# Kernel optimization log

Measured on AMD Instinct MI355X. Metric: run time of the kernel, lower is better.

## Reference

```python
import jax, jax.numpy as jnp
import numpy as np

B, S, D, H = 2, 4096, 512, 8
HD = D // H  # 64


def setup_inputs() -> dict:
    key = jax.random.key(0)
    ks = jax.random.split(key, 9)
    def lin_init(kw, kb, fan_in, fan_out):
        bound = 1.0 / np.sqrt(fan_in)
        W = jax.random.uniform(kw, (fan_in, fan_out), minval=-bound, maxval=bound, dtype=jnp.float32)
        b = jax.random.uniform(kb, (fan_out,), minval=-bound, maxval=bound, dtype=jnp.float32)
        return W, b
    Wq, bq = lin_init(ks[0], ks[1], D, D)
    Wk, bk = lin_init(ks[2], ks[3], D, D)
    Wv, bv = lin_init(ks[4], ks[5], D, D)
    query = jax.random.normal(ks[6], (B, S, D), dtype=jnp.float32)
    key_in = jax.random.normal(ks[7], (B, S, D), dtype=jnp.float32)
    value = jax.random.normal(ks[8], (B, S, D), dtype=jnp.float32)
    return {"query": query, "key": key_in, "value": value,
            "Wq": Wq, "bq": bq, "Wk": Wk, "bk": bk, "Wv": Wv, "bv": bv}


def _split_heads(x):
    # [B, S, D] -> [B, H, S, HD]
    b, s, _ = x.shape
    return x.reshape(b, s, H, HD).transpose(0, 2, 1, 3)


def reference(query, key, value, Wq, bq, Wk, bk, Wv, bv):
    Q = _split_heads(query @ Wq + bq)
    K = _split_heads(key @ Wk + bk)
    V = _split_heads(value @ Wv + bv)
    scale = 1.0 / np.sqrt(HD).astype(np.float32)
    # scores: [B, H, Sq, Sk]
    scores = jnp.einsum('bhqd,bhkd->bhqk', Q, K) * scale
    weights = jax.nn.softmax(scores, axis=-1)
    att = jnp.einsum('bhqk,bhkd->bhqd', weights, V)
    # [B, H, S, HD] -> [B, S, D]
    return att.transpose(0, 2, 1, 3).reshape(query.shape[0], query.shape[1], D)
```

## Files before the change

### kernel.cpp

```cpp
#include <hip/hip_runtime.h>
#include <hip/hip_bf16.h>
#include <cstdint>


typedef __bf16   bf16x8 __attribute__((ext_vector_type(8)));
typedef _Float16 f16x8  __attribute__((ext_vector_type(8)));
typedef _Float16 f16x2  __attribute__((ext_vector_type(2)));
typedef float    f32x4  __attribute__((ext_vector_type(4)));
typedef float    f32x16 __attribute__((ext_vector_type(16)));
typedef unsigned int   u32;
typedef unsigned int   u32x4 __attribute__((ext_vector_type(4)));
typedef unsigned short u16;

#define NB  2
#define SEQ 4096
#define DIM 512
#define NH  8
#define HD  64
#define WSZ (DIM * DIM)
#define XSZ (NB * SEQ * DIM)
#define QSZ (NB * NH * SEQ * HD)

#if __has_builtin(__builtin_amdgcn_fdot2)
#define HAVE_FDOT2 1
#else
#define HAVE_FDOT2 0
#endif

__device__ __forceinline__ u16 f2bf(float f) {
    __bf16 h = (__bf16)f; return __builtin_bit_cast(u16, h);
}
__device__ __forceinline__ u16 f2h(float f) {
    _Float16 h = (_Float16)f; return __builtin_bit_cast(u16, h);
}
__device__ __forceinline__ u32 pack_pkrtz(float a, float b) {
    auto pk = __builtin_amdgcn_cvt_pkrtz(a, b);
    return __builtin_bit_cast(u32, pk);
}
__device__ __forceinline__ bf16x8 cvt8p(float4 a, float4 b) {
    bf16x8 o;
    o[0]=(__bf16)a.x; o[1]=(__bf16)a.y; o[2]=(__bf16)a.z; o[3]=(__bf16)a.w;
    o[4]=(__bf16)b.x; o[5]=(__bf16)b.y; o[6]=(__bf16)b.z; o[7]=(__bf16)b.w;
    return o;
}
__device__ __forceinline__ void dma16(const u16* g, u16* l) {
    __builtin_amdgcn_global_load_lds(
        (const __attribute__((address_space(1))) u32*)g,
        (__attribute__((address_space(3))) u32*)l, 16, 0, 0);
}

__global__ __launch_bounds__(256) void prep_kernel(
    const float* __restrict__ xq, const float* __restrict__ xk,
    const float* __restrict__ xv,
    const float* __restrict__ Wq, const float* __restrict__ Wk,
    const float* __restrict__ Wv,
    u16* __restrict__ xb, u16* __restrict__ wtImg)
{
    __shared__ u16 lT[64 * 65];
    const int id = blockIdx.x;
    const int t = threadIdx.x;
    if (id < 3072) {
        const int p = id >> 10, rest = id & 1023;
        const int mtile = rest >> 4, kk = rest & 15;
        const float* X = (p == 0) ? xq : ((p == 1) ? xk : xv);
        const int row = t >> 1, half = t & 1;
        const float* src = X + ((size_t)(mtile * 128 + row)) * DIM + kk * 32 + half * 16;
        u16* dst = xb + (size_t)p * XSZ + ((size_t)(mtile * 16 + kk)) * 4096 + row * 32;
        const int sr = (row ^ (row >> 2)) & 3;
        float4 a0 = ((const float4*)src)[0], a1 = ((const float4*)src)[1];
        float4 a2 = ((const float4*)src)[2], a3 = ((const float4*)src)[3];
        const int c0 = (half * 2) ^ sr, c1 = (half * 2 + 1) ^ sr;
        *(bf16x8*)(dst + (c0 << 3)) = cvt8p(a0, a1);
        *(bf16x8*)(dst + (c1 << 3)) = cvt8p(a2, a3);
    } else {
        const int id2 = id - 3072;
        const int p = id2 >> 6;
        const float* W = (p == 0) ? Wq : ((p == 1) ? Wk : Wv);
        const int r0 = ((id2 >> 3) & 7) * 64, c0 = (id2 & 7) * 64;
#pragma unroll
        for (int i = 0; i < 16; i++) {
            int idx = i * 256 + t, rowk = idx >> 6, coln = idx & 63;
            lT[coln * 65 + rowk] = f2bf(W[(size_t)(r0 + rowk) * DIM + c0 + coln]);
        }
        __syncthreads();
#pragma unroll
        for (int i = 0; i < 2; i++) {
            const int idx = i * 256 + t;
            const int nl = idx >> 3, ch = idx & 7;
            const int n = c0 + nl;
            const int row = n & 127, ntile = n >> 7;
            const int kk = (r0 >> 5) + (ch >> 2);
            const int sw = (ch & 3) ^ ((row ^ (row >> 2)) & 3);
            u16* d = wtImg + (size_t)p * WSZ + ((size_t)(ntile * 16 + kk)) * 4096
                   + row * 32 + (sw << 3);
#pragma unroll
            for (int e = 0; e < 8; e++) d[e] = lT[nl * 65 + ch * 8 + e];
        }
    }
}

__global__ __launch_bounds__(256) void proj_kernel(
    const u16* __restrict__ xb, const u16* __restrict__ wtImg,
    const float* __restrict__ bq, const float* __restrict__ bk,
    const float* __restrict__ bv,
    u16* __restrict__ qb, u16* __restrict__ kbImg, u16* __restrict__ vtImg)
{
    __shared__ u16 smem[16384];

    const int tid = threadIdx.x;
    const int wave = tid >> 6, lane = tid & 63;
    const int l16 = lane & 15, quad = lane >> 4;
    const int wq = wave >> 1, wn = wave & 1;

    const int id = blockIdx.x;
    const int xcd = id & 7, j = id >> 3;
    const int p = j >> 5, t5 = j & 31;
    int mb, nb;
    if (p < 2) { mb = xcd * 8 + (t5 >> 2); nb = t5 & 3; }
    else       { nb = xcd * 8 + (t5 >> 2); mb = t5 & 3; }

    const u16* Abase = (p < 2) ? xb + (size_t)p * XSZ + (size_t)mb * 16 * 4096
                               : wtImg + (size_t)2 * WSZ + (size_t)mb * 16 * 4096;
    const u16* Bbase = (p < 2) ? wtImg + (size_t)p * WSZ + (size_t)nb * 16 * 4096
                               : xb + (size_t)2 * XSZ + (size_t)nb * 16 * 4096;
    const int doff = tid * 8;

    f32x4 acc[4][4];
#pragma unroll
    for (int ms = 0; ms < 4; ms++)
#pragma unroll
        for (int ns = 0; ns < 4; ns++)
#pragma unroll
            for (int jj = 0; jj < 4; jj++) acc[ms][ns][jj] = 0.f;

#pragma unroll
    for (int e = 0; e < 2; e++) {
        dma16(Abase + e * 2048 + doff, smem + e * 2048 + doff);
        dma16(Bbase + e * 2048 + doff, smem + 4096 + e * 2048 + doff);
    }
    Abase += 4096; Bbase += 4096;

    for (int kt = 0; kt < 16; kt++) {
        __syncthreads();
        if (kt < 15) {
            u16* lb = smem + ((kt + 1) & 1) * 8192;
#pragma unroll
            for (int e = 0; e < 2; e++) {
                dma16(Abase + e * 2048 + doff, lb + e * 2048 + doff);
                dma16(Bbase + e * 2048 + doff, lb + 4096 + e * 2048 + doff);
            }
            Abase += 4096; Bbase += 4096;
        }
        const u16* lA = smem + (kt & 1) * 8192;
        const u16* lB = lA + 4096;

        bf16x8 af[4];
#pragma unroll
        for (int ms = 0; ms < 4; ms++) {
            const int row = wq * 64 + ms * 16 + l16;
            const int sr = (row ^ (row >> 2)) & 3;
            af[ms] = *(const bf16x8*)&lA[row * 32 + ((quad ^ sr) << 3)];
        }
#pragma unroll
        for (int ns = 0; ns < 4; ns++) {
            const int rowb = wn * 64 + ns * 16 + l16;
            const int sb = (rowb ^ (rowb >> 2)) & 3;
            const bf16x8 b = *(const bf16x8*)&lB[rowb * 32 + ((quad ^ sb) << 3)];
#pragma unroll
            for (int ms = 0; ms < 4; ms++)
                acc[ms][ns] = __builtin_amdgcn_mfma_f32_16x16x32_bf16(af[ms], b, acc[ms][ns], 0, 0, 0);
        }
    }

    __syncthreads();
    if (p < 2) {
        const float* bias = p ? bk : bq;
        const float cs = (p == 0) ? 0.18033688011112042f : 1.0f;
        const int stl = wn * 2 + wq;
        const int hh = nb * 2 + wn;
#pragma unroll
        for (int ns = 0; ns < 4; ns++) {
            const int ch = ns * 16 + l16;
            const float bval = bias[hh * 64 + ch];
#pragma unroll
            for (int ms = 0; ms < 4; ms++)
#pragma unroll
                for (int rr = 0; rr < 4; rr++) {
                    const int sqL = ms * 16 + quad * 4 + rr;
                    const float v = (acc[ms][ns][rr] + bval) * cs;
                    int off;
                    if (p == 0) off = sqL * 64 + ch;
                    else        off = sqL * 64 +
                                      (((ch >> 3) ^ ((sqL ^ (sqL >> 3)) & 7)) << 3) + (ch & 7);
                    smem[stl * 4096 + off] = f2bf(v);
                }
        }
    } else {
        const int stl = wq * 2 + wn;
#pragma unroll
        for (int ms = 0; ms < 4; ms++)
#pragma unroll
            for (int rr = 0; rr < 4; rr++) {
                const int hd = ms * 16 + quad * 4 + rr;
                const float bval = bv[mb * 128 + wq * 64 + hd];
                const int swh = (hd ^ (hd >> 3)) & 7;
#pragma unroll
                for (int ns = 0; ns < 4; ns++) {
                    const int nl = ns * 16 + l16;
                    const int sqpL = (nl & ~12) | ((nl & 8) >> 1) | ((nl & 4) << 1);
                    smem[stl * 4096 + hd * 64 +
                         (((sqpL >> 3) ^ swh) << 3) + (sqpL & 7)] =
                        f2h(acc[ms][ns][rr] + bval);
                }
            }
    }
    __syncthreads();

    {
        u16* dstp; size_t gbase;
        if (p < 2) {
            const int hh = nb * 2 + (wave >> 1);
            const int b2 = mb >> 5;
            const int row0 = (mb * 128 + (wave & 1) * 64) & 4095;
            if (p == 0) { dstp = qb;    gbase = ((size_t)(b2 * NH + hh) * 4096 + row0) * 64; }
            else        { dstp = kbImg; gbase = ((size_t)((b2 * NH + hh) * 64 + (row0 >> 6))) * 4096; }
        } else {
            const int hh = mb * 2 + (wave >> 1);
            const int b2 = nb >> 5;
            const int nblk = (nb & 31) * 2 + (wave & 1);
            dstp = vtImg; gbase = ((size_t)((b2 * NH + hh) * 64 + nblk)) * 4096;
        }
#pragma unroll
        for (int e = 0; e < 8; e++) {
            const u32x4 vv = *(const u32x4*)&smem[wave * 4096 + e * 512 + lane * 8];
            *(u32x4*)(dstp + gbase + e * 512 + lane * 8) = vv;
        }
    }
}

__global__ __launch_bounds__(512, 4) void attn_kernel(
    const u16* __restrict__ qb, const u16* __restrict__ kbImg,
    const u16* __restrict__ vtImg, float* __restrict__ out)
{
    __shared__ u16 smem[2 * 4 * 4096];
    float* cmb = (float*)smem;

    const int tid = threadIdx.x;
    const int wave = tid >> 6, lane = tid & 63;
    const int m31 = lane & 31, h = lane >> 5;
    const int wq = wave >> 1, kh = wave & 1;

    const int blk = blockIdx.x;
    const int xcd = blk & 7, idx = blk >> 3;
    const int bh = xcd * 2 + (idx >> 5);
    const int qt = idx & 31;
    const int qbase = qt * 128 + wq * 32;

    bf16x8 qF[4];
#pragma unroll
    for (int c = 0; c < 4; c++)
        qF[c] = *(const bf16x8*)(qb + ((size_t)bh * SEQ + qbase + m31) * HD + c * 16 + h * 8);

    f32x16 O0, O1;
#pragma unroll
    for (int j = 0; j < 16; j++) { O0[j] = 0.f; O1[j] = 0.f; }
    float la_ = 0.f, lb_ = 0.f;
#if HAVE_FDOT2
    const f16x2 one2 = {(_Float16)1.f, (_Float16)1.f};
#endif

    const int st  = wave >> 1;
    const int hw  = wave & 1;
    const u16* img = (st & 1) ? vtImg : kbImg;
    const u16* gp = img + ((size_t)(bh * 64 + (st >> 1) * 32)) * 4096 + hw * 2048 + lane * 8;
    {
        u16* lb = smem + st * 4096 + hw * 2048 + lane * 8;
#pragma unroll
        for (int e = 0; e < 4; e++) dma16(gp + e * 512, lb + e * 512);
        gp += 4096;
    }

    const int swV0 = (m31 ^ (m31 >> 3)) & 7;
    const int rV1  = 32 + m31;
    const int swV1 = (rV1 ^ (rV1 >> 3)) & 7;
    const int rK0  = m31;
    const int swK0 = (rK0 ^ (rK0 >> 3)) & 7;
    const int rK1  = 32 + m31;
    const int swK1 = (rK1 ^ (rK1 >> 3)) & 7;

    const int NT = 32;
    for (int it = 0; it < NT; it++) {
        __syncthreads();
        if (it + 1 < NT) {
            u16* lb = smem + ((((it + 1) & 1) * 4 + st)) * 4096 + hw * 2048 + lane * 8;
#pragma unroll
            for (int e = 0; e < 4; e++) dma16(gp + e * 512, lb + e * 512);
            gp += 4096;
        }
        const u16* sK = smem + (size_t)(((it & 1) * 4) + kh * 2) * 4096;
        const u16* sV = sK + 4096;

        bf16x8 kA0[4];
#pragma unroll
        for (int c = 0; c < 4; c++)
            kA0[c] = *(const bf16x8*)&sK[(rK0 << 6) + (((2 * c + h) ^ swK0) << 3)];

        f32x16 Sv0;
#pragma unroll
        for (int j = 0; j < 16; j++) Sv0[j] = 0.f;
        __builtin_amdgcn_s_setprio(1);
#pragma unroll
        for (int c = 0; c < 4; c++)
            Sv0 = __builtin_amdgcn_mfma_f32_32x32x16_bf16(kA0[c], qF[c], Sv0, 0, 0, 0);
        __builtin_amdgcn_s_setprio(0);

        f16x8 vA00[2], vA01[2];
#pragma unroll
        for (int c2 = 0; c2 < 2; c2++) {
            vA00[c2] = *(const f16x8*)&sV[(m31 << 6) + (((2 * c2 + h) ^ swV0) << 3)];
            vA01[c2] = *(const f16x8*)&sV[(rV1 << 6) + (((2 * c2 + h) ^ swV1) << 3)];
        }

        u32 P0[8];
#pragma unroll
        for (int mm = 0; mm < 8; mm++) {
            const float ea = __builtin_amdgcn_exp2f(Sv0[2 * mm]);
            const float eb = __builtin_amdgcn_exp2f(Sv0[2 * mm + 1]);
            P0[mm] = pack_pkrtz(ea, eb);
#if HAVE_FDOT2
            const f16x2 pp = __builtin_bit_cast(f16x2, P0[mm]);
            if (mm & 1) lb_ = __builtin_amdgcn_fdot2(pp, one2, lb_, false);
            else        la_ = __builtin_amdgcn_fdot2(pp, one2, la_, false);
#else
            if (mm & 1) lb_ += ea + eb; else la_ += ea + eb;
#endif
        }
        u32x4 g0, g1;
        g0[0] = P0[0]; g0[1] = P0[1]; g0[2] = P0[2]; g0[3] = P0[3];
        g1[0] = P0[4]; g1[1] = P0[5]; g1[2] = P0[6]; g1[3] = P0[7];
        const f16x8 pf00 = __builtin_bit_cast(f16x8, g0);
        const f16x8 pf01 = __builtin_bit_cast(f16x8, g1);

        bf16x8 kA1[4];
#pragma unroll
        for (int c = 0; c < 4; c++)
            kA1[c] = *(const bf16x8*)&sK[(rK1 << 6) + (((2 * c + h) ^ swK1) << 3)];

        f32x16 Sv1;
#pragma unroll
        for (int j = 0; j < 16; j++) Sv1[j] = 0.f;

        __builtin_amdgcn_s_setprio(1);
        Sv1 = __builtin_amdgcn_mfma_f32_32x32x16_bf16(kA1[0], qF[0], Sv1, 0, 0, 0);
        O0  = __builtin_amdgcn_mfma_f32_32x32x16_f16(vA00[0], pf00, O0, 0, 0, 0);
        Sv1 = __builtin_amdgcn_mfma_f32_32x32x16_bf16(kA1[1], qF[1], Sv1, 0, 0, 0);
        O0  = __builtin_amdgcn_mfma_f32_32x32x16_f16(vA00[1], pf01, O0, 0, 0, 0);
        Sv1 = __builtin_amdgcn_mfma_f32_32x32x16_bf16(kA1[2], qF[2], Sv1, 0, 0, 0);
        O1  = __builtin_amdgcn_mfma_f32_32x32x16_f16(vA01[0], pf00, O1, 0, 0, 0);
        Sv1 = __builtin_amdgcn_mfma_f32_32x32x16_bf16(kA1[3], qF[3], Sv1, 0, 0, 0);
        O1  = __builtin_amdgcn_mfma_f32_32x32x16_f16(vA01[1], pf01, O1, 0, 0, 0);
        __builtin_amdgcn_s_setprio(0);

        f16x8 vA10[2], vA11[2];
#pragma unroll
        for (int c2 = 0; c2 < 2; c2++) {
            vA10[c2] = *(const f16x8*)&sV[(m31 << 6) + (((4 + 2 * c2 + h) ^ swV0) << 3)];
            vA11[c2] = *(const f16x8*)&sV[(rV1 << 6) + (((4 + 2 * c2 + h) ^ swV1) << 3)];
        }

        u32 P1[8];
#pragma unroll
        for (int mm = 0; mm < 8; mm++) {
            const float ea = __builtin_amdgcn_exp2f(Sv1[2 * mm]);
            const float eb = __builtin_amdgcn_exp2f(Sv1[2 * mm + 1]);
            P1[mm] = pack_pkrtz(ea, eb);
#if HAVE_FDOT2
            const f16x2 pp = __builtin_bit_cast(f16x2, P1[mm]);
            if (mm & 1) lb_ = __builtin_amdgcn_fdot2(pp, one2, lb_, false);
            else        la_ = __builtin_amdgcn_fdot2(pp, one2, la_, false);
#else
            if (mm & 1) lb_ += ea + eb; else la_ += ea + eb;
#endif
        }
        u32x4 h0, h1;
        h0[0] = P1[0]; h0[1] = P1[1]; h0[2] = P1[2]; h0[3] = P1[3];
        h1[0] = P1[4]; h1[1] = P1[5]; h1[2] = P1[6]; h1[3] = P1[7];
        const f16x8 pf10 = __builtin_bit_cast(f16x8, h0);
        const f16x8 pf11 = __builtin_bit_cast(f16x8, h1);

        __builtin_amdgcn_s_setprio(1);
        O0 = __builtin_amdgcn_mfma_f32_32x32x16_f16(vA10[0], pf10, O0, 0, 0, 0);
        O0 = __builtin_amdgcn_mfma_f32_32x32x16_f16(vA10[1], pf11, O0, 0, 0, 0);
        O1 = __builtin_amdgcn_mfma_f32_32x32x16_f16(vA11[0], pf10, O1, 0, 0, 0);
        O1 = __builtin_amdgcn_mfma_f32_32x32x16_f16(vA11[1], pf11, O1, 0, 0, 0);
        __builtin_amdgcn_s_setprio(0);
    }

    float l_acc = la_ + lb_;
    l_acc += __shfl_xor(l_acc, 32);
    __syncthreads();
    if (kh == 1) {
#pragma unroll
        for (int hg = 0; hg < 2; hg++)
#pragma unroll
            for (int mm = 0; mm < 4; mm++) {
                f32x4 o;
#pragma unroll
                for (int j = 0; j < 4; j++) o[j] = (hg ? O1 : O0)[4 * mm + j];
                *(f32x4*)&cmb[(((wq * 2 + hg) * 4 + mm) << 8) + lane * 4] = o;
            }
        cmb[8192 + wq * 64 + lane] = l_acc;
    }
    __syncthreads();

    if (kh == 0) {
        const int b = bh >> 3, hcol = bh & 7;
        const float lt = l_acc + cmb[8192 + wq * 64 + lane];
        const float inv = 1.0f / lt;
        const int sq = qbase + m31;
#pragma unroll
        for (int hg = 0; hg < 2; hg++)
#pragma unroll
            for (int mm = 0; mm < 4; mm++) {
                const f32x4 po = *(const f32x4*)&cmb[(((wq * 2 + hg) * 4 + mm) << 8) + lane * 4];
                f32x4 o;
#pragma unroll
                for (int j = 0; j < 4; j++)
                    o[j] = ((hg ? O1 : O0)[4 * mm + j] + po[j]) * inv;
                *(f32x4*)&out[(((size_t)(b * SEQ + sq)) << 9) + hcol * 64
                              + hg * 32 + 8 * mm + 4 * h] = o;
            }
    }
}

extern "C" void kernel_launch(void* const* d_in, const int* in_sizes, int n_in,
                              void* d_out, int out_size, void* d_ws, size_t ws_size,
                              hipStream_t stream)
{
    const float* q  = (const float*)d_in[0];
    const float* k  = (const float*)d_in[1];
    const float* v  = (const float*)d_in[2];
    const float* Wq = (const float*)d_in[3];
    const float* bq = (const float*)d_in[4];
    const float* Wk = (const float*)d_in[5];
    const float* bk = (const float*)d_in[6];
    const float* Wv = (const float*)d_in[7];
    const float* bv = (const float*)d_in[8];
    float* out = (float*)d_out;

    u16* xb  = (u16*)d_ws;
    u16* wti = xb  + (size_t)3 * XSZ;
    u16* qbp = wti + (size_t)3 * WSZ;
    u16* kbp = qbp + (size_t)QSZ;
    u16* vtp = kbp + (size_t)QSZ;

    prep_kernel<<<dim3(3264), 256, 0, stream>>>(q, k, v, Wq, Wk, Wv, xb, wti);
    proj_kernel<<<dim3(768),  256, 0, stream>>>(xb, wti, bq, bk, bv,
                                                qbp, kbp, vtp);
    attn_kernel<<<dim3(512),  512, 0, stream>>>(qbp, kbp, vtp, out);
}
```

Before: 202.5 us.

## Fuse fp32-to-bf16 activation conversion into projection GEMM loads

The prep kernel no longer converts the three fp32 activation tensors to a swizzled bf16 image in workspace. The projection kernel now reads fp32 activations directly with register loads, converts them, and writes them into LDS after the MFMA work of each k-step, while weights still stream in via global_load_lds DMA. This removes a full write-then-read round trip of the bf16 activation copy and shrinks the prep launch to the weight transpose only. In exchange, the GEMM loop reads twice as many bytes for activations, holds more registers, and does conversion work inside the loop.

```diff
diff --git a/kernel.cpp b/kernel.cpp
--- a/kernel.cpp
+++ b/kernel.cpp
@@ -18,7 +18,6 @@
 #define NH  8
 #define HD  64
 #define WSZ (DIM * DIM)
-#define XSZ (NB * SEQ * DIM)
 #define QSZ (NB * NH * SEQ * HD)
 
 #if __has_builtin(__builtin_amdgcn_fdot2)
@@ -49,58 +48,39 @@
         (__attribute__((address_space(3))) u32*)l, 16, 0, 0);
 }
 
-__global__ __launch_bounds__(256) void prep_kernel(
-    const float* __restrict__ xq, const float* __restrict__ xk,
-    const float* __restrict__ xv,
+__global__ __launch_bounds__(256) void wt_kernel(
     const float* __restrict__ Wq, const float* __restrict__ Wk,
-    const float* __restrict__ Wv,
-    u16* __restrict__ xb, u16* __restrict__ wtImg)
+    const float* __restrict__ Wv, u16* __restrict__ wtImg)
 {
     __shared__ u16 lT[64 * 65];
-    const int id = blockIdx.x;
+    const int p = blockIdx.z;
+    const float* W = (p == 0) ? Wq : ((p == 1) ? Wk : Wv);
+    const int r0 = blockIdx.x * 64, c0 = blockIdx.y * 64;
     const int t = threadIdx.x;
-    if (id < 3072) {
-        const int p = id >> 10, rest = id & 1023;
-        const int mtile = rest >> 4, kk = rest & 15;
-        const float* X = (p == 0) ? xq : ((p == 1) ? xk : xv);
-        const int row = t >> 1, half = t & 1;
-        const float* src = X + ((size_t)(mtile * 128 + row)) * DIM + kk * 32 + half * 16;
-        u16* dst = xb + (size_t)p * XSZ + ((size_t)(mtile * 16 + kk)) * 4096 + row * 32;
-        const int sr = (row ^ (row >> 2)) & 3;
-        float4 a0 = ((const float4*)src)[0], a1 = ((const float4*)src)[1];
-        float4 a2 = ((const float4*)src)[2], a3 = ((const float4*)src)[3];
-        const int c0 = (half * 2) ^ sr, c1 = (half * 2 + 1) ^ sr;
-        *(bf16x8*)(dst + (c0 << 3)) = cvt8p(a0, a1);
-        *(bf16x8*)(dst + (c1 << 3)) = cvt8p(a2, a3);
-    } else {
-        const int id2 = id - 3072;
-        const int p = id2 >> 6;
-        const float* W = (p == 0) ? Wq : ((p == 1) ? Wk : Wv);
-        const int r0 = ((id2 >> 3) & 7) * 64, c0 = (id2 & 7) * 64;
-#pragma unroll
-        for (int i = 0; i < 16; i++) {
-            int idx = i * 256 + t, rowk = idx >> 6, coln = idx & 63;
-            lT[coln * 65 + rowk] = f2bf(W[(size_t)(r0 + rowk) * DIM + c0 + coln]);
-        }
-        __syncthreads();
-#pragma unroll
-        for (int i = 0; i < 2; i++) {
-            const int idx = i * 256 + t;
-            const int nl = idx >> 3, ch = idx & 7;
-            const int n = c0 + nl;
-            const int row = n & 127, ntile = n >> 7;
-            const int kk = (r0 >> 5) + (ch >> 2);
-            const int sw = (ch & 3) ^ ((row ^ (row >> 2)) & 3);
-            u16* d = wtImg + (size_t)p * WSZ + ((size_t)(ntile * 16 + kk)) * 4096
-                   + row * 32 + (sw << 3);
-#pragma unroll
-            for (int e = 0; e < 8; e++) d[e] = lT[nl * 65 + ch * 8 + e];
-        }
+#pragma unroll
+    for (int i = 0; i < 16; i++) {
+        int idx = i * 256 + t, rowk = idx >> 6, coln = idx & 63;
+        lT[coln * 65 + rowk] = f2bf(W[(size_t)(r0 + rowk) * DIM + c0 + coln]);
+    }
+    __syncthreads();
+#pragma unroll
+    for (int i = 0; i < 2; i++) {
+        const int idx = i * 256 + t;
+        const int nl = idx >> 3, ch = idx & 7;
+        const int n = c0 + nl;
+        const int row = n & 127, ntile = n >> 7;
+        const int kk = (r0 >> 5) + (ch >> 2);
+        const int sw = (ch & 3) ^ ((row ^ (row >> 2)) & 3);
+        u16* d = wtImg + (size_t)p * WSZ + ((size_t)(ntile * 16 + kk)) * 4096
+               + row * 32 + (sw << 3);
+#pragma unroll
+        for (int e = 0; e < 8; e++) d[e] = lT[nl * 65 + ch * 8 + e];
     }
 }
 
 __global__ __launch_bounds__(256) void proj_kernel(
-    const u16* __restrict__ xb, const u16* __restrict__ wtImg,
+    const float* __restrict__ xq, const float* __restrict__ xk,
+    const float* __restrict__ xv, const u16* __restrict__ wtImg,
     const float* __restrict__ bq, const float* __restrict__ bk,
     const float* __restrict__ bv,
     u16* __restrict__ qb, u16* __restrict__ kbImg, u16* __restrict__ vtImg)
@@ -119,10 +99,17 @@
     if (p < 2) { mb = xcd * 8 + (t5 >> 2); nb = t5 & 3; }
     else       { nb = xcd * 8 + (t5 >> 2); mb = t5 & 3; }
 
-    const u16* Abase = (p < 2) ? xb + (size_t)p * XSZ + (size_t)mb * 16 * 4096
+    const float* Xp = (p == 0) ? xq : ((p == 1) ? xk : xv);
+    const int xtile = (p < 2) ? mb : nb;
+    const int row = tid >> 1, half = tid & 1;
+    const int sr = (row ^ (row >> 2)) & 3;
+    const float* xsrc = Xp + (size_t)(xtile * 128 + row) * DIM + half * 16;
+    const int xldsoff = (p < 2) ? 0 : 4096;
+    const int c0 = (((half * 2) ^ sr) << 3), c1 = (((half * 2 + 1) ^ sr) << 3);
+
+    const u16* Wbase = (p < 2) ? wtImg + (size_t)p * WSZ + (size_t)nb * 16 * 4096
                                : wtImg + (size_t)2 * WSZ + (size_t)mb * 16 * 4096;
-    const u16* Bbase = (p < 2) ? wtImg + (size_t)p * WSZ + (size_t)nb * 16 * 4096
-                               : xb + (size_t)2 * XSZ + (size_t)nb * 16 * 4096;
+    const int wldsoff = (p < 2) ? 4096 : 0;
     const int doff = tid * 8;
 
     f32x4 acc[4][4];
@@ -133,23 +120,31 @@
 #pragma unroll
             for (int jj = 0; jj < 4; jj++) acc[ms][ns][jj] = 0.f;
 
-#pragma unroll
-    for (int e = 0; e < 2; e++) {
-        dma16(Abase + e * 2048 + doff, smem + e * 2048 + doff);
-        dma16(Bbase + e * 2048 + doff, smem + 4096 + e * 2048 + doff);
-    }
-    Abase += 4096; Bbase += 4096;
+    {
+        float4 a0 = ((const float4*)xsrc)[0], a1 = ((const float4*)xsrc)[1];
+        float4 a2 = ((const float4*)xsrc)[2], a3 = ((const float4*)xsrc)[3];
+        xsrc += 32;
+#pragma unroll
+        for (int e = 0; e < 2; e++)
+            dma16(Wbase + e * 2048 + doff, smem + wldsoff + e * 2048 + doff);
+        Wbase += 4096;
+        u16* xd = smem + xldsoff + row * 32;
+        *(bf16x8*)(xd + c0) = cvt8p(a0, a1);
+        *(bf16x8*)(xd + c1) = cvt8p(a2, a3);
+    }
 
     for (int kt = 0; kt < 16; kt++) {
         __syncthreads();
+        float4 a0, a1, a2, a3;
         if (kt < 15) {
-            u16* lb = smem + ((kt + 1) & 1) * 8192;
-#pragma unroll
-            for (int e = 0; e < 2; e++) {
-                dma16(Abase + e * 2048 + doff, lb + e * 2048 + doff);
-                dma16(Bbase + e * 2048 + doff, lb + 4096 + e * 2048 + doff);
-            }
-            Abase += 4096; Bbase += 4096;
+            u16* buf = smem + ((kt + 1) & 1) * 8192;
+#pragma unroll
+            for (int e = 0; e < 2; e++)
+                dma16(Wbase + e * 2048 + doff, buf + wldsoff + e * 2048 + doff);
+            Wbase += 4096;
+            a0 = ((const float4*)xsrc)[0]; a1 = ((const float4*)xsrc)[1];
+            a2 = ((const float4*)xsrc)[2]; a3 = ((const float4*)xsrc)[3];
+            xsrc += 32;
         }
         const u16* lA = smem + (kt & 1) * 8192;
         const u16* lB = lA + 4096;
@@ -157,9 +152,9 @@
         bf16x8 af[4];
 #pragma unroll
         for (int ms = 0; ms < 4; ms++) {
-            const int row = wq * 64 + ms * 16 + l16;
-            const int sr = (row ^ (row >> 2)) & 3;
-            af[ms] = *(const bf16x8*)&lA[row * 32 + ((quad ^ sr) << 3)];
+            const int rowa = wq * 64 + ms * 16 + l16;
+            const int sra = (rowa ^ (rowa >> 2)) & 3;
+            af[ms] = *(const bf16x8*)&lA[rowa * 32 + ((quad ^ sra) << 3)];
         }
 #pragma unroll
         for (int ns = 0; ns < 4; ns++) {
@@ -169,6 +164,12 @@
 #pragma unroll
             for (int ms = 0; ms < 4; ms++)
                 acc[ms][ns] = __builtin_amdgcn_mfma_f32_16x16x32_bf16(af[ms], b, acc[ms][ns], 0, 0, 0);
+        }
+
+        if (kt < 15) {
+            u16* xd = smem + ((kt + 1) & 1) * 8192 + xldsoff + row * 32;
+            *(bf16x8*)(xd + c0) = cvt8p(a0, a1);
+            *(bf16x8*)(xd + c1) = cvt8p(a2, a3);
         }
     }
 
@@ -448,14 +449,13 @@
     const float* bv = (const float*)d_in[8];
     float* out = (float*)d_out;
 
-    u16* xb  = (u16*)d_ws;
-    u16* wti = xb  + (size_t)3 * XSZ;
+    u16* wti = (u16*)d_ws;
     u16* qbp = wti + (size_t)3 * WSZ;
     u16* kbp = qbp + (size_t)QSZ;
     u16* vtp = kbp + (size_t)QSZ;
 
-    prep_kernel<<<dim3(3264), 256, 0, stream>>>(q, k, v, Wq, Wk, Wv, xb, wti);
-    proj_kernel<<<dim3(768),  256, 0, stream>>>(xb, wti, bq, bk, bv,
-                                                qbp, kbp, vtp);
-    attn_kernel<<<dim3(512),  512, 0, stream>>>(qbp, kbp, vtp, out);
-}
+    wt_kernel  <<<dim3(8, 8, 3), 256, 0, stream>>>(Wq, Wk, Wv, wti);
+    proj_kernel<<<dim3(768),     256, 0, stream>>>(q, k, v, wti, bq, bk, bv,
+                                                   qbp, kbp, vtp);
+    attn_kernel<<<dim3(512),     512, 0, stream>>>(qbp, kbp, vtp, out);
+}
```

New measurement: 205.8 us (median of 3 runs). No clear change (+1.6%).
